# Optimization experiments

Hardware: AMD Instinct MI355X
Metric: run time of the kernel (lower is better)

The kernel has to match this reference:

```python
import jax, jax.numpy as jnp
import numpy as np

B, H, W, C = 16, 32, 32, 256
N = H * W


def setup_inputs() -> dict:
    key = jax.random.key(0)
    ks = jax.random.split(key, 8)
    x = jax.random.normal(ks[0], (B, H, W, C), dtype=jnp.float32)
    # nn.LazyLinear(C): weight (C, C), bias (C,)
    scale = 1.0 / np.sqrt(C)
    Wq = jax.random.uniform(ks[1], (C, C), jnp.float32, -scale, scale)
    bq = jax.random.uniform(ks[2], (C,), jnp.float32, -scale, scale)
    Wk = jax.random.uniform(ks[3], (C, C), jnp.float32, -scale, scale)
    bk = jax.random.uniform(ks[4], (C,), jnp.float32, -scale, scale)
    Wv = jax.random.uniform(ks[5], (C, C), jnp.float32, -scale, scale)
    bv = jax.random.uniform(ks[6], (C,), jnp.float32, -scale, scale)
    # torch.randn(H, H*W, W)
    Wp = jax.random.normal(ks[7], (H, N, W), dtype=jnp.float32)
    return {"x": x, "Wq": Wq, "bq": bq, "Wk": Wk, "bk": bk,
            "Wv": Wv, "bv": bv, "Wp": Wp}


def reference(x, Wq, bq, Wk, bk, Wv, bv, Wp):
    b, h, w, c = x.shape
    n = h * w
    # Linear projections (torch Linear: x @ W^T + b), flatten spatial dims to N tokens
    q = (jnp.einsum('bhwc,dc->bhwd', x, Wq) + bq).reshape(b, n, c)
    k = (jnp.einsum('bhwc,dc->bhwd', x, Wk) + bk).reshape(b, n, c)
    v = (jnp.einsum('bhwc,dc->bhwd', x, Wv) + bv).reshape(b, n, c)
    # Unscaled attention over the N spatial tokens (no 1/sqrt(C) in the original)
    scores = jnp.einsum('bnc,bmc->bnm', q, k)          # (B, N, N)
    attn = jax.nn.softmax(scores, axis=-1)
    qkv = jnp.einsum('bnm,bmc->bnc', attn, v)           # (B, N, C)
    # z = (qkv^T [B,1,C,N] @ Wp [H,N,W]).transpose(-2,-1) -> (B, H, W, C)
    z = jnp.einsum('bnc,hnw->bhwc', qkv, Wp)
    return z
```

## Files before the change

### kernel.cpp

```cpp
#include <hip/hip_runtime.h>
#include <hip/hip_bf16.h>

#define BB 16
#define NN 1024
#define CC 256

typedef __attribute__((ext_vector_type(8))) short bf16x8;
typedef __attribute__((ext_vector_type(4))) float f32x4;

#define GPTR(p) ((const __attribute__((address_space(1))) void*)(p))
#define LPTR(p) ((__attribute__((address_space(3))) void*)(p))

__device__ __forceinline__ unsigned short f2bf(float f) {
  union { float f; unsigned u; } v; v.f = f;
  unsigned r = v.u + 0x7FFFu + ((v.u >> 16) & 1u);
  return (unsigned short)(r >> 16);
}

__global__ void cast_kernel(const float* __restrict__ src,
                            unsigned short* __restrict__ dst, int n) {
  int i = blockIdx.x * blockDim.x + threadIdx.x;
  if (i < n) dst[i] = f2bf(src[i]);
}

__global__ __launch_bounds__(256) void wp_transpose(const float* __restrict__ Wp,
                                                    unsigned short* __restrict__ Amat) {
  __shared__ float tile[32][33];
  int h = blockIdx.y;
  int n0 = blockIdx.x * 32;
#pragma unroll
  for (int j = 0; j < 4; j++) {
    int idx = threadIdx.x + j * 256;
    int a = idx >> 5, wc = idx & 31;
    tile[a][wc] = Wp[(size_t)h * (NN * 32) + (size_t)(n0 + a) * 32 + wc];
  }
  __syncthreads();
#pragma unroll
  for (int j = 0; j < 4; j++) {
    int idx = threadIdx.x + j * 256;
    int wc = idx >> 5, a = idx & 31;
    Amat[(size_t)(h * 32 + wc) * NN + n0 + a] = f2bf(tile[a][wc]);
  }
}

template <int BIAS_MODE, int F32OUT>
__global__ __launch_bounds__(256) void gemm_tile(
    const unsigned short* __restrict__ A, int lda, long sA,
    const unsigned short* __restrict__ Bt, int ldb, long sB,
    const float* __restrict__ bias,
    void* __restrict__ Out, int ldo, long sO, int K) {
  __shared__ unsigned short As[2 * 128 * 32];
  __shared__ unsigned short Bs[2 * 64 * 32];
  int b = blockIdx.z;
  int m0 = blockIdx.x * 128;
  int n0 = blockIdx.y * 64;
  int t = threadIdx.x;
  int w = t >> 6, lane = t & 63;
  int wm = (w >> 1) * 64, wn = (w & 1) * 32;
  int r = lane & 15, g = lane >> 4;

  const unsigned short* Ab = A + (long)b * sA;
  const unsigned short* Bb = Bt + (long)b * sB;

  int srow = t >> 2;
  int scol = (t & 3) * 8;

  f32x4 acc[4][2];
#pragma unroll
  for (int i = 0; i < 4; i++)
#pragma unroll
    for (int j = 0; j < 2; j++) acc[i][j] = (f32x4){0.f, 0.f, 0.f, 0.f};

  for (int k0 = 0; k0 < K; k0 += 64) {
    __syncthreads();
#pragma unroll
    for (int kh = 0; kh < 2; kh++) {
#pragma unroll
      for (int jj = 0; jj < 2; jj++) {
        __builtin_amdgcn_global_load_lds(
            GPTR(Ab + (long)(m0 + srow + jj * 64) * lda + k0 + kh * 32 + scol),
            LPTR(&As[kh * 4096 + jj * 2048 + t * 8]), 16, 0, 0);
      }
      __builtin_amdgcn_global_load_lds(
          GPTR(Bb + (long)(n0 + srow) * ldb + k0 + kh * 32 + scol),
          LPTR(&Bs[kh * 2048 + t * 8]), 16, 0, 0);
    }
    __syncthreads();
#pragma unroll
    for (int kh = 0; kh < 2; kh++) {
      bf16x8 af[4], bfr[2];
#pragma unroll
      for (int ti = 0; ti < 4; ti++)
        af[ti] = *(const bf16x8*)&As[kh * 4096 + (wm + ti * 16 + r) * 32 + g * 8];
#pragma unroll
      for (int tj = 0; tj < 2; tj++)
        bfr[tj] = *(const bf16x8*)&Bs[kh * 2048 + (wn + tj * 16 + r) * 32 + g * 8];
#pragma unroll
      for (int ti = 0; ti < 4; ti++)
#pragma unroll
        for (int tj = 0; tj < 2; tj++)
          acc[ti][tj] = __builtin_amdgcn_mfma_f32_16x16x32_bf16(af[ti], bfr[tj], acc[ti][tj], 0, 0, 0);
    }
  }

#pragma unroll
  for (int ti = 0; ti < 4; ti++) {
#pragma unroll
    for (int tj = 0; tj < 2; tj++) {
      int col = n0 + wn + tj * 16 + r;
      float bc = (BIAS_MODE == 1) ? bias[col] : 0.0f;
#pragma unroll
      for (int rr = 0; rr < 4; rr++) {
        int row = m0 + wm + ti * 16 + g * 4 + rr;
        float val = acc[ti][tj][rr] + bc;
        if (BIAS_MODE == 2) val += bias[row];
        long oidx = (long)b * sO + (long)row * ldo + col;
        if (F32OUT)
          ((float*)Out)[oidx] = val;
        else
          ((unsigned short*)Out)[oidx] = f2bf(val);
      }
    }
  }
}

#define PS_LD 1032
__global__ __launch_bounds__(512, 4) void attn_fused(
    const unsigned short* __restrict__ Q,
    const unsigned short* __restrict__ Km,
    const unsigned short* __restrict__ Vt,
    unsigned short* __restrict__ QKVt) {
  __shared__ unsigned short ShBuf[32 * PS_LD];
  __shared__ float red[4][2][16];
  int b = blockIdx.y;
  int n0 = blockIdx.x * 32;
  int t = threadIdx.x;
  int w = t >> 6, lane = t & 63;
  int rg = w >> 2, ch = w & 3;
  int r = lane & 15, g = lane >> 4;

  const unsigned short* qbase = Q + ((long)b * NN + n0 + rg * 16 + r) * CC + g * 8;
  bf16x8 qf[8];
#pragma unroll
  for (int kk = 0; kk < 8; kk++) qf[kk] = *(const bf16x8*)(qbase + kk * 32);

  const unsigned short* kbase = Km + (long)b * NN * CC;
  int strow = t >> 2;
  int stcol = (t & 3) * 8;

  f32x4 acc[16];
#pragma unroll
  for (int tt = 0; tt < 16; tt++) acc[tt] = (f32x4){0.f, 0.f, 0.f, 0.f};

  for (int kk = 0; kk < 8; kk++) {
    __syncthreads();
#pragma unroll
    for (int jj = 0; jj < 8; jj++) {
      __builtin_amdgcn_global_load_lds(
          GPTR(kbase + (long)(strow + jj * 128) * CC + kk * 32 + stcol),
          LPTR(&ShBuf[(strow + jj * 128) * 32 + stcol]), 16, 0, 0);
    }
    __syncthreads();
#pragma unroll
    for (int tt = 0; tt < 16; tt++) {
      bf16x8 bv = *(const bf16x8*)&ShBuf[(ch * 256 + tt * 16 + r) * 32 + g * 8];
      acc[tt] = __builtin_amdgcn_mfma_f32_16x16x32_bf16(qf[kk], bv, acc[tt], 0, 0, 0);
    }
  }

  float mrow[4];
#pragma unroll
  for (int rr = 0; rr < 4; rr++) {
    float m = acc[0][rr];
#pragma unroll
    for (int tt = 1; tt < 16; tt++) m = fmaxf(m, acc[tt][rr]);
#pragma unroll
    for (int d = 1; d < 16; d <<= 1) m = fmaxf(m, __shfl_xor(m, d, 64));
    mrow[rr] = m;
  }
  if (r == 0) {
#pragma unroll
    for (int rr = 0; rr < 4; rr++) red[ch][rg][g * 4 + rr] = mrow[rr];
  }
  __syncthreads();
#pragma unroll
  for (int rr = 0; rr < 4; rr++) {
    float m = red[0][rg][g * 4 + rr];
#pragma unroll
    for (int c2 = 1; c2 < 4; c2++) m = fmaxf(m, red[c2][rg][g * 4 + rr]);
    mrow[rr] = m;
  }
  __syncthreads();
  float ssum[4];
#pragma unroll
  for (int rr = 0; rr < 4; rr++) {
    float s = 0.f;
#pragma unroll
    for (int tt = 0; tt < 16; tt++) {
      float e = exp2f((acc[tt][rr] - mrow[rr]) * 1.44269504088896f);
      acc[tt][rr] = e;
      s += e;
    }
#pragma unroll
    for (int d = 1; d < 16; d <<= 1) s += __shfl_xor(s, d, 64);
    ssum[rr] = s;
  }
  if (r == 0) {
#pragma unroll
    for (int rr = 0; rr < 4; rr++) red[ch][rg][g * 4 + rr] = ssum[rr];
  }
  __syncthreads();
#pragma unroll
  for (int rr = 0; rr < 4; rr++) {
    float s = red[0][rg][g * 4 + rr] + red[1][rg][g * 4 + rr] +
              red[2][rg][g * 4 + rr] + red[3][rg][g * 4 + rr];
    float inv = 1.0f / s;
    int prow = rg * 16 + g * 4 + rr;
#pragma unroll
    for (int tt = 0; tt < 16; tt++) {
      ShBuf[prow * PS_LD + ch * 256 + tt * 16 + r] = f2bf(acc[tt][rr] * inv);
    }
  }
  __syncthreads();

  const unsigned short* vbase = Vt + (long)b * NN * CC;
  int cw = w * 32;
  f32x4 o[2][2];
#pragma unroll
  for (int i = 0; i < 2; i++)
#pragma unroll
    for (int j = 0; j < 2; j++) o[i][j] = (f32x4){0.f, 0.f, 0.f, 0.f};

  for (int m0 = 0; m0 < NN; m0 += 32) {
    bf16x8 ar[2], br[2];
#pragma unroll
    for (int bt = 0; bt < 2; bt++)
      br[bt] = *(const bf16x8*)(vbase + (long)(cw + bt * 16 + r) * NN + m0 + g * 8);
#pragma unroll
    for (int rt = 0; rt < 2; rt++)
      ar[rt] = *(const bf16x8*)&ShBuf[(rt * 16 + r) * PS_LD + m0 + g * 8];
#pragma unroll
    for (int rt = 0; rt < 2; rt++)
#pragma unroll
      for (int bt = 0; bt < 2; bt++)
        o[rt][bt] = __builtin_amdgcn_mfma_f32_16x16x32_bf16(ar[rt], br[bt], o[rt][bt], 0, 0, 0);
  }

  unsigned short* obase = QKVt + (long)b * NN * CC;
#pragma unroll
  for (int rt = 0; rt < 2; rt++) {
#pragma unroll
    for (int bt = 0; bt < 2; bt++) {
      int c = cw + bt * 16 + r;
#pragma unroll
      for (int rr = 0; rr < 4; rr++) {
        int n = n0 + rt * 16 + g * 4 + rr;
        obase[(long)c * NN + n] = f2bf(o[rt][bt][rr]);
      }
    }
  }
}

extern "C" void kernel_launch(void* const* d_in, const int* in_sizes, int n_in,
                              void* d_out, int out_size, void* d_ws, size_t ws_size,
                              hipStream_t stream) {
  const float* x  = (const float*)d_in[0];
  const float* Wq = (const float*)d_in[1];
  const float* bq = (const float*)d_in[2];
  const float* Wk = (const float*)d_in[3];
  const float* bk = (const float*)d_in[4];
  const float* Wv = (const float*)d_in[5];
  const float* bv = (const float*)d_in[6];
  const float* Wp = (const float*)d_in[7];
  float* out = (float*)d_out;

  const long BNC = (long)BB * NN * CC;

  char* p = (char*)d_ws;
  unsigned short* xb   = (unsigned short*)p; p += BNC * 2;
  unsigned short* wqb  = (unsigned short*)p; p += CC * CC * 2;
  unsigned short* wkb  = (unsigned short*)p; p += CC * CC * 2;
  unsigned short* wvb  = (unsigned short*)p; p += CC * CC * 2;
  unsigned short* Amat = (unsigned short*)p; p += (long)NN * NN * 2;
  unsigned short* Qb   = (unsigned short*)p; p += BNC * 2;
  unsigned short* Kb   = (unsigned short*)p; p += BNC * 2;
  unsigned short* Vtb  = (unsigned short*)p; p += BNC * 2;
  unsigned short* QKVt = (unsigned short*)p; p += BNC * 2;

  cast_kernel<<<(int)((BNC + 255) / 256), 256, 0, stream>>>(x, xb, (int)BNC);
  cast_kernel<<<(CC * CC + 255) / 256, 256, 0, stream>>>(Wq, wqb, CC * CC);
  cast_kernel<<<(CC * CC + 255) / 256, 256, 0, stream>>>(Wk, wkb, CC * CC);
  cast_kernel<<<(CC * CC + 255) / 256, 256, 0, stream>>>(Wv, wvb, CC * CC);
  wp_transpose<<<dim3(NN / 32, 32), 256, 0, stream>>>(Wp, Amat);

  gemm_tile<1, 0><<<dim3(8, 4, BB), 256, 0, stream>>>(
      xb, CC, (long)NN * CC, wqb, CC, 0L, bq, Qb, CC, (long)NN * CC, CC);
  gemm_tile<1, 0><<<dim3(8, 4, BB), 256, 0, stream>>>(
      xb, CC, (long)NN * CC, wkb, CC, 0L, bk, Kb, CC, (long)NN * CC, CC);
  gemm_tile<2, 0><<<dim3(2, 16, BB), 256, 0, stream>>>(
      wvb, CC, 0L, xb, CC, (long)NN * CC, bv, Vtb, NN, (long)NN * CC, CC);

  attn_fused<<<dim3(NN / 32, BB), 512, 0, stream>>>(Qb, Kb, Vtb, QKVt);

  gemm_tile<0, 1><<<dim3(8, 4, BB), 256, 0, stream>>>(
      Amat, NN, 0L, QKVt, NN, (long)NN * CC, nullptr,
      out, CC, (long)NN * CC, NN);
}
```

Before: 186.7 us.

## Fuse QKV projections into one GEMM, merge casts, swizzle attention LDS

Merges the four cast launches into one kernel that also packs the three biases, and replaces the three separate Q/K/V projection GEMMs with a single GEMM over a concatenated 768-wide weight, writing V transposed in its epilogue. In the attention kernel, the padded P buffer is replaced with an XOR-swizzled layout to avoid LDS bank conflicts, and the PV loop is unrolled. This cuts launch count, reads x once per tile instead of three times, and lowers shared memory per block. The transposed V store in the epilogue is strided, which may cost write efficiency.

```diff
diff --git a/kernel.cpp b/kernel.cpp
--- a/kernel.cpp
+++ b/kernel.cpp
@@ -17,10 +17,29 @@
   return (unsigned short)(r >> 16);
 }
 
-__global__ void cast_kernel(const float* __restrict__ src,
-                            unsigned short* __restrict__ dst, int n) {
+__global__ void cast_all(const float* __restrict__ x,
+                         const float* __restrict__ Wq, const float* __restrict__ Wk,
+                         const float* __restrict__ Wv,
+                         const float* __restrict__ bq, const float* __restrict__ bk,
+                         const float* __restrict__ bv,
+                         unsigned short* __restrict__ xb,
+                         unsigned short* __restrict__ wqkvb,
+                         float* __restrict__ bqkv) {
+  const int NX = BB * NN * CC;
+  const int NW = CC * CC;
   int i = blockIdx.x * blockDim.x + threadIdx.x;
-  if (i < n) dst[i] = f2bf(src[i]);
+  if (i < NX) { xb[i] = f2bf(x[i]); return; }
+  int j = i - NX;
+  if (j < 3 * NW) {
+    const float* w = (j < NW) ? Wq : (j < 2 * NW ? Wk : Wv);
+    wqkvb[j] = f2bf(w[j % NW]);
+    return;
+  }
+  int jj = j - 3 * NW;
+  if (jj < 3 * CC) {
+    const float* bb = (jj < CC) ? bq : (jj < 2 * CC ? bk : bv);
+    bqkv[jj] = bb[jj % CC];
+  }
 }
 
 __global__ __launch_bounds__(256) void wp_transpose(const float* __restrict__ Wp,
@@ -113,7 +132,6 @@
       for (int rr = 0; rr < 4; rr++) {
         int row = m0 + wm + ti * 16 + g * 4 + rr;
         float val = acc[ti][tj][rr] + bc;
-        if (BIAS_MODE == 2) val += bias[row];
         long oidx = (long)b * sO + (long)row * ldo + col;
         if (F32OUT)
           ((float*)Out)[oidx] = val;
@@ -124,13 +142,92 @@
   }
 }
 
-#define PS_LD 1032
+__global__ __launch_bounds__(256) void gemm_qkv(
+    const unsigned short* __restrict__ A,
+    const unsigned short* __restrict__ Bt,
+    const float* __restrict__ bias,
+    unsigned short* __restrict__ Qb, unsigned short* __restrict__ Kb,
+    unsigned short* __restrict__ Vtb) {
+  __shared__ unsigned short As[2 * 128 * 32];
+  __shared__ unsigned short Bs[2 * 64 * 32];
+  int b = blockIdx.z;
+  int m0 = blockIdx.x * 128;
+  int n0 = blockIdx.y * 64;
+  int t = threadIdx.x;
+  int w = t >> 6, lane = t & 63;
+  int wm = (w >> 1) * 64, wn = (w & 1) * 32;
+  int r = lane & 15, g = lane >> 4;
+
+  const unsigned short* Ab = A + (long)b * NN * CC;
+  int srow = t >> 2;
+  int scol = (t & 3) * 8;
+
+  f32x4 acc[4][2];
+#pragma unroll
+  for (int i = 0; i < 4; i++)
+#pragma unroll
+    for (int j = 0; j < 2; j++) acc[i][j] = (f32x4){0.f, 0.f, 0.f, 0.f};
+
+  for (int k0 = 0; k0 < CC; k0 += 64) {
+    __syncthreads();
+#pragma unroll
+    for (int kh = 0; kh < 2; kh++) {
+#pragma unroll
+      for (int jj = 0; jj < 2; jj++) {
+        __builtin_amdgcn_global_load_lds(
+            GPTR(Ab + (long)(m0 + srow + jj * 64) * CC + k0 + kh * 32 + scol),
+            LPTR(&As[kh * 4096 + jj * 2048 + t * 8]), 16, 0, 0);
+      }
+      __builtin_amdgcn_global_load_lds(
+          GPTR(Bt + (long)(n0 + srow) * CC + k0 + kh * 32 + scol),
+          LPTR(&Bs[kh * 2048 + t * 8]), 16, 0, 0);
+    }
+    __syncthreads();
+#pragma unroll
+    for (int kh = 0; kh < 2; kh++) {
+      bf16x8 af[4], bfr[2];
+#pragma unroll
+      for (int ti = 0; ti < 4; ti++)
+        af[ti] = *(const bf16x8*)&As[kh * 4096 + (wm + ti * 16 + r) * 32 + g * 8];
+#pragma unroll
+      for (int tj = 0; tj < 2; tj++)
+        bfr[tj] = *(const bf16x8*)&Bs[kh * 2048 + (wn + tj * 16 + r) * 32 + g * 8];
+#pragma unroll
+      for (int ti = 0; ti < 4; ti++)
+#pragma unroll
+        for (int tj = 0; tj < 2; tj++)
+          acc[ti][tj] = __builtin_amdgcn_mfma_f32_16x16x32_bf16(af[ti], bfr[tj], acc[ti][tj], 0, 0, 0);
+    }
+  }
+
+  int seg = n0 >> 8;
+  unsigned short* QK = (seg == 0) ? Qb : Kb;
+#pragma unroll
+  for (int ti = 0; ti < 4; ti++) {
+#pragma unroll
+    for (int tj = 0; tj < 2; tj++) {
+      int col = n0 + wn + tj * 16 + r;
+      int c = col & 255;
+      float bc = bias[col];
+#pragma unroll
+      for (int rr = 0; rr < 4; rr++) {
+        int row = m0 + wm + ti * 16 + g * 4 + rr;
+        float val = acc[ti][tj][rr] + bc;
+        if (seg < 2)
+          QK[(long)b * NN * CC + (long)row * CC + c] = f2bf(val);
+        else
+          Vtb[(long)b * NN * CC + (long)c * NN + row] = f2bf(val);
+      }
+    }
+  }
+}
+
 __global__ __launch_bounds__(512, 4) void attn_fused(
     const unsigned short* __restrict__ Q,
     const unsigned short* __restrict__ Km,
     const unsigned short* __restrict__ Vt,
     unsigned short* __restrict__ QKVt) {
-  __shared__ unsigned short ShBuf[32 * PS_LD];
+  __shared__ unsigned short ShBuf[32 * 1024];
   __shared__ float red[4][2][16];
   int b = blockIdx.y;
   int n0 = blockIdx.x * 32;
@@ -216,9 +313,12 @@
               red[2][rg][g * 4 + rr] + red[3][rg][g * 4 + rr];
     float inv = 1.0f / s;
     int prow = rg * 16 + g * 4 + rr;
+    int sw = prow & 7;
 #pragma unroll
     for (int tt = 0; tt < 16; tt++) {
-      ShBuf[prow * PS_LD + ch * 256 + tt * 16 + r] = f2bf(acc[tt][rr] * inv);
+      int col = ch * 256 + tt * 16 + r;
+      int chunk = (col >> 3) ^ sw;
+      ShBuf[prow * 1024 + chunk * 8 + (col & 7)] = f2bf(acc[tt][rr] * inv);
     }
   }
   __syncthreads();
@@ -231,14 +331,18 @@
 #pragma unroll
     for (int j = 0; j < 2; j++) o[i][j] = (f32x4){0.f, 0.f, 0.f, 0.f};
 
+#pragma unroll 4
   for (int m0 = 0; m0 < NN; m0 += 32) {
     bf16x8 ar[2], br[2];
 #pragma unroll
     for (int bt = 0; bt < 2; bt++)
       br[bt] = *(const bf16x8*)(vbase + (long)(cw + bt * 16 + r) * NN + m0 + g * 8);
 #pragma unroll
-    for (int rt = 0; rt < 2; rt++)
-      ar[rt] = *(const bf16x8*)&ShBuf[(rt * 16 + r) * PS_LD + m0 + g * 8];
+    for (int rt = 0; rt < 2; rt++) {
+      int prow = rt * 16 + r;
+      int chunk = ((m0 >> 3) + g) ^ (prow & 7);
+      ar[rt] = *(const bf16x8*)&ShBuf[prow * 1024 + chunk * 8];
+    }
 #pragma unroll
     for (int rt = 0; rt < 2; rt++)
 #pragma unroll
@@ -277,28 +381,21 @@
   const long BNC = (long)BB * NN * CC;
 
   char* p = (char*)d_ws;
-  unsigned short* xb   = (unsigned short*)p; p += BNC * 2;
-  unsigned short* wqb  = (unsigned short*)p; p += CC * CC * 2;
-  unsigned short* wkb  = (unsigned short*)p; p += CC * CC * 2;
-  unsigned short* wvb  = (unsigned short*)p; p += CC * CC * 2;
-  unsigned short* Amat = (unsigned short*)p; p += (long)NN * NN * 2;
-  unsigned short* Qb   = (unsigned short*)p; p += BNC * 2;
-  unsigned short* Kb   = (unsigned short*)p; p += BNC * 2;
-  unsigned short* Vtb  = (unsigned short*)p; p += BNC * 2;
-  unsigned short* QKVt = (unsigned short*)p; p += BNC * 2;
-
-  cast_kernel<<<(int)((BNC + 255) / 256), 256, 0, stream>>>(x, xb, (int)BNC);
-  cast_kernel<<<(CC * CC + 255) / 256, 256, 0, stream>>>(Wq, wqb, CC * CC);
-  cast_kernel<<<(CC * CC + 255) / 256, 256, 0, stream>>>(Wk, wkb, CC * CC);
-  cast_kernel<<<(CC * CC + 255) / 256, 256, 0, stream>>>(Wv, wvb, CC * CC);
+  unsigned short* xb    = (unsigned short*)p; p += BNC * 2;
+  unsigned short* wqkvb = (unsigned short*)p; p += 3L * CC * CC * 2;
+  float*          bqkv  = (float*)p;          p += 4096;
+  unsigned short* Amat  = (unsigned short*)p; p += (long)NN * NN * 2;
+  unsigned short* Qb    = (unsigned short*)p; p += BNC * 2;
+  unsigned short* Kb    = (unsigned short*)p; p += BNC * 2;
+  unsigned short* Vtb   = (unsigned short*)p; p += BNC * 2;
+  unsigned short* QKVt  = (unsigned short*)p; p += BNC * 2;
+
+  const long TOT = BNC + 3L * CC * CC + 3 * CC;
+  cast_all<<<(int)((TOT + 255) / 256), 256, 0, stream>>>(
+      x, Wq, Wk, Wv, bq, bk, bv, xb, wqkvb, bqkv);
   wp_transpose<<<dim3(NN / 32, 32), 256, 0, stream>>>(Wp, Amat);
 
-  gemm_tile<1, 0><<<dim3(8, 4, BB), 256, 0, stream>>>(
-      xb, CC, (long)NN * CC, wqb, CC, 0L, bq, Qb, CC, (long)NN * CC, CC);
-  gemm_tile<1, 0><<<dim3(8, 4, BB), 256, 0, stream>>>(
-      xb, CC, (long)NN * CC, wkb, CC, 0L, bk, Kb, CC, (long)NN * CC, CC);
-  gemm_tile<2, 0><<<dim3(2, 16, BB), 256, 0, stream>>>(
-      wvb, CC, 0L, xb, CC, (long)NN * CC, bv, Vtb, NN, (long)NN * CC, CC);
+  gemm_qkv<<<dim3(8, 12, BB), 256, 0, stream>>>(xb, wqkvb, bqkv, Qb, Kb, Vtb);
 
   attn_fused<<<dim3(NN / 32, BB), 512, 0, stream>>>(Qb, Kb, Vtb, QKVt);
 
```

Result: faster. 181.0 us (-3.0%).
